# Optimization experiments

Measured on AMD Instinct MI355X. Metric: run time of the kernel, lower is better.

Reference implementation:

```python
import jax, jax.numpy as jnp
import numpy as np
from jax import lax

S = 2          # scale_factor
K = 5          # k_reassembly
KK = K * K     # 25 reassembly weights per output pixel


def _conv2d(x, w, b, pad):
    y = lax.conv_general_dilated(x, w, (1, 1), [(pad, pad), (pad, pad)],
                                 dimension_numbers=('NCHW', 'OIHW', 'NCHW'))
    return y + b[None, :, None, None]


def _pixel_shuffle(x, r):
    # (N, C*r*r, H, W) -> (N, C, H*r, W*r), torch PixelShuffle semantics
    n, crr, h, w = x.shape
    c = crr // (r * r)
    x = x.reshape(n, c, r, r, h, w)
    x = x.transpose(0, 1, 4, 2, 5, 3)
    return x.reshape(n, c, h * r, w * r)


def setup_inputs() -> dict:
    key = jax.random.key(0)
    k1, k2, k3 = jax.random.split(key, 3)
    x = jax.random.normal(k1, (4, 256, 64, 64), dtype=jnp.float32)
    w_comp = jax.random.normal(k2, (64, 256, 1, 1), dtype=jnp.float32) * 0.05
    b_comp = jnp.zeros((64,), dtype=jnp.float32)
    w_enc = jax.random.normal(k3, (S * S * KK, 64, 3, 3), dtype=jnp.float32) * 0.05
    b_enc = jnp.zeros((S * S * KK,), dtype=jnp.float32)
    return {"x": x, "w_comp": w_comp, "b_comp": b_comp, "w_enc": w_enc, "b_enc": b_enc}


def reference(x, w_comp, b_comp, w_enc, b_enc):
    N, C, H, W = x.shape
    p = K // 2
    # kernel prediction branch
    compressed = _conv2d(x, w_comp, b_comp, pad=0)                 # (N, 64, H, W)
    kernels = _conv2d(compressed, w_enc, b_enc, pad=1)             # (N, S*S*KK, H, W)
    kernels = _pixel_shuffle(kernels, S)                           # (N, KK, H*S, W*S)
    kernels = jax.nn.softmax(kernels, axis=1)
    # regroup kernels: (N, KK, Hs, Ws) -> (N, H, W, KK, S*S)  (torch unfold order: kh then kw)
    k_unf = kernels.reshape(N, KK, H, S, W, S)
    k_unf = k_unf.transpose(0, 2, 4, 1, 3, 5).reshape(N, H, W, KK, S * S)
    # gather KxK input patches: (N, C, H, W, KK), flattened (ih, iw) with ih outer
    xp = jnp.pad(x, ((0, 0), (0, 0), (p, p), (p, p)))
    patches = jnp.stack([xp[:, :, i:i + H, j:j + W]
                         for i in range(K) for j in range(K)], axis=-1)
    # weighted reassembly: per-pixel (C, KK) @ (KK, S*S)
    out = jnp.einsum('nchwk,nhwkq->nhwcq', patches, k_unf)          # (N, H, W, C, S*S)
    out = out.reshape(N, H, W, C * S * S).transpose(0, 3, 1, 2)     # (N, C*S*S, H, W)
    return _pixel_shuffle(out, S)                                   # (N, C, H*S, W*S)
```

## Files before the change

kernel.cpp:

```cpp
#include <hip/hip_runtime.h>
#include <hip/hip_fp16.h>

#define NB 4
#define CI 256
#define HH 64
#define WW 64
#define MC 64
#define HS 128
#define WS_ 128
#define HW 4096

typedef __attribute__((ext_vector_type(8))) short short8v;
typedef __attribute__((ext_vector_type(4))) float floatx4;

__device__ inline unsigned short f2bf(float f) {
  union { float f; unsigned u; } v; v.f = f;
  unsigned r = v.u + 0x7FFFu + ((v.u >> 16) & 1u);
  return (unsigned short)(r >> 16);
}

__global__ __launch_bounds__(256) void prep_kernel(
    const float* __restrict__ w_comp, const float* __restrict__ w_enc,
    unsigned short* __restrict__ Aw1, unsigned short* __restrict__ Aw2) {
  int i = blockIdx.x * 256 + threadIdx.x;
  if (i < 16384) {
    int kl = i & 31, o = (i >> 5) & 63, ks = i >> 11;
    Aw1[i] = f2bf(w_comp[o * 256 + ks * 32 + kl]);
  } else if (i < 16384 + 64512) {
    int j = i - 16384;
    int kl = j & 31, o = (j >> 5) % 112, ks = (j >> 5) / 112;
    int t = ks >> 1, m = (ks & 1) * 32 + kl;
    Aw2[j] = (o < 100) ? f2bf(w_enc[o * 576 + m * 9 + t]) : (unsigned short)0;
  }
}

__global__ __launch_bounds__(512, 1) void conv1x1_mfma(
    const float* __restrict__ x, const unsigned short* __restrict__ Aw1,
    const float* __restrict__ b_comp, unsigned short* __restrict__ comp_cl) {
  __shared__ float pacc[2][64][49];
  int tid = threadIdx.x;
  int wid = tid >> 6, lane = tid & 63;
  int tileid = wid & 1, kh = wid >> 1;
  int Nt = blockIdx.x * 2 + tileid;
  int n = Nt >> 8, pixbase = (Nt & 255) * 16;
  int l15 = lane & 15, g = lane >> 4;
  int pix = pixbase + l15;

  floatx4 acc[4];
#pragma unroll
  for (int ot = 0; ot < 4; ++ot) acc[ot] = (floatx4){0.f, 0.f, 0.f, 0.f};

  const float* xb = x + (size_t)n * CI * HW + pix;
  const unsigned short* ab = Aw1 + l15 * 32 + g * 8;

#pragma unroll
  for (int s = 0; s < 2; ++s) {
    int ks = kh * 2 + s;
    int c0 = ks * 32 + g * 8;
    short8v bfrag;
#pragma unroll
    for (int j = 0; j < 8; ++j)
      bfrag[j] = (short)f2bf(xb[(size_t)(c0 + j) * HW]);
#pragma unroll
    for (int ot = 0; ot < 4; ++ot) {
      short8v af = *(const short8v*)(ab + (ks * 64 + ot * 16) * 32);
      acc[ot] = __builtin_amdgcn_mfma_f32_16x16x32_bf16(af, bfrag, acc[ot], 0, 0, 0);
    }
  }

  if (kh > 0) {
#pragma unroll
    for (int ot = 0; ot < 4; ++ot)
#pragma unroll
      for (int r = 0; r < 4; ++r)
        pacc[tileid][lane][(kh - 1) * 16 + ot * 4 + r] = acc[ot][r];
  }
  __syncthreads();
  if (kh == 0) {
    unsigned short* cp = comp_cl + ((size_t)(n * HW + pix)) * 64;
#pragma unroll
    for (int ot = 0; ot < 4; ++ot) {
      const float4 bv = *(const float4*)(b_comp + ot * 16 + g * 4);
      float v0 = acc[ot][0] + bv.x, v1 = acc[ot][1] + bv.y;
      float v2 = acc[ot][2] + bv.z, v3 = acc[ot][3] + bv.w;
#pragma unroll
      for (int sl = 0; sl < 3; ++sl) {
        v0 += pacc[tileid][lane][sl * 16 + ot * 4 + 0];
        v1 += pacc[tileid][lane][sl * 16 + ot * 4 + 1];
        v2 += pacc[tileid][lane][sl * 16 + ot * 4 + 2];
        v3 += pacc[tileid][lane][sl * 16 + ot * 4 + 3];
      }
      unsigned h01 = (unsigned)f2bf(v0) | ((unsigned)f2bf(v1) << 16);
      unsigned h23 = (unsigned)f2bf(v2) | ((unsigned)f2bf(v3) << 16);
      *(int2*)(cp + ot * 16 + g * 4) = make_int2((int)h01, (int)h23);
    }
  }
}

#define TAPP(W, V, fa, fb)                                                     \
  asm("v_fma_mix_f32 %0, %1, %2, %0 op_sel:[0,0,0] op_sel_hi:[1,0,0]"          \
      : "+v"(a00) : "v"(W), "v"(fa));                                          \
  asm("v_fma_mix_f32 %0, %1, %2, %0 op_sel:[1,0,0] op_sel_hi:[1,0,0]"          \
      : "+v"(a01) : "v"(W), "v"(fa));                                          \
  asm("v_fma_mix_f32 %0, %1, %2, %0 op_sel:[0,0,0] op_sel_hi:[1,0,0]"          \
      : "+v"(a10) : "v"(V), "v"(fb));                                          \
  asm("v_fma_mix_f32 %0, %1, %2, %0 op_sel:[1,0,0] op_sel_hi:[1,0,0]"          \
      : "+v"(a11) : "v"(V), "v"(fb));

#define ROWP(WA, WB, WC, WD, WE, VA, VB, VC, VD, VE, RP)                       \
  { const float* rr = (RP);                                                    \
    float2 f01 = *(const float2*)(rr);                                         \
    float2 f23 = *(const float2*)(rr + 2);                                     \
    float2 f45 = *(const float2*)(rr + 4);                                     \
    TAPP(WA, VA, f01.x, f01.y) TAPP(WB, VB, f01.y, f23.x)                      \
    TAPP(WC, VC, f23.x, f23.y) TAPP(WD, VD, f23.y, f45.x)                      \
    TAPP(WE, VE, f45.x, f45.y) }

__device__ __forceinline__ float4 load_slot20(const float* __restrict__ xb,
                                              int h0, int w0, int f,
                                              bool interior) {
  int c = f / 30, rem = f - c * 30, r = rem / 5, h = rem - r * 5;
  int gh = h0 - 2 + r, gw = w0 - 2 + h * 4;
  if (interior) {
    const float* gp = xb + (size_t)c * HW + gh * WW + gw;
    float2 lo = *(const float2*)gp;
    float2 hi = *(const float2*)(gp + 2);
    return make_float4(lo.x, lo.y, hi.x, hi.y);
  }
  int ghc = min(max(gh, 0), 63);
  const float* rowp = xb + (size_t)c * HW + ghc * WW;
  float v0 = rowp[min(max(gw + 0, 0), 63)];
  float v1 = rowp[min(max(gw + 1, 0), 63)];
  float v2 = rowp[min(max(gw + 2, 0), 63)];
  float v3 = rowp[min(max(gw + 3, 0), 63)];
  bool rok = ((unsigned)gh < 64u);
  v0 = (rok && (unsigned)(gw + 0) < 64u) ? v0 : 0.f;
  v1 = (rok && (unsigned)(gw + 1) < 64u) ? v1 : 0.f;
  v2 = (rok && (unsigned)(gw + 2) < 64u) ? v2 : 0.f;
  v3 = (rok && (unsigned)(gw + 3) < 64u) ? v3 : 0.f;
  return make_float4(v0, v1, v2, v3);
}

__global__ __launch_bounds__(512, 4) void fused_kernel(
    const float* __restrict__ x,
    const unsigned short* __restrict__ comp_cl,
    const unsigned short* __restrict__ Aw2,
    const float* __restrict__ b_enc,
    float* __restrict__ out) {
  __shared__ float smem[12672];
  float* paccF = smem;
  float* xp = smem;
  unsigned int* wlds = (unsigned int*)(smem + 10880);

  int tid = threadIdx.x;
  int bid = blockIdx.x;
  int tile = bid & 127, n = bid >> 7;
  int tyi = tile >> 2, txi = tile & 3;
  int ty0 = tyi * 4, tx0 = txi * 32;
  int h0 = tyi * 2, w0 = txi * 16;

  int wid = tid >> 6, lane = tid & 63;
  int tileid = wid & 1, kh = wid >> 1;
  int l15 = lane & 15, g = lane >> 4;

  {
    int pix = (h0 + tileid) * 64 + w0 + l15;
    int y = pix >> 6, xcol = pix & 63;

    bool vm[9];
    int sh9[9];
#pragma unroll
    for (int t = 0; t < 9; ++t) {
      int dy = t / 3, dx = t % 3;
      vm[t] = ((unsigned)(y + dy - 1) < 64u) && ((unsigned)(xcol + dx - 1) < 64u);
      sh9[t] = (dy - 1) * 64 + (dx - 1);
    }

    floatx4 acc[7];
#pragma unroll
    for (int ot = 0; ot < 7; ++ot) acc[ot] = (floatx4){0.f, 0.f, 0.f, 0.f};

    const unsigned short* cb = comp_cl + (size_t)n * HW * 64;
    const unsigned short* ab = Aw2 + l15 * 32 + g * 8;
    const short8v zv = {0, 0, 0, 0, 0, 0, 0, 0};

    int ks0 = (kh < 2) ? kh * 5 : 10 + (kh - 2) * 4;
    int len = (kh < 2) ? 5 : 4;
#pragma unroll
    for (int s = 0; s < 5; ++s) {
      if (s < len) {
        int ks = ks0 + s;
        int t = ks >> 1, mh = ks & 1;
        const unsigned short* bp = cb + (pix + sh9[t]) * 64 + mh * 32 + g * 8;
        short8v bfrag = vm[t] ? *(const short8v*)bp : zv;
#pragma unroll
        for (int ot = 0; ot < 7; ++ot) {
          short8v af = *(const short8v*)(ab + (ks * 112 + ot * 16) * 32);
          acc[ot] = __builtin_amdgcn_mfma_f32_16x16x32_bf16(af, bfrag, acc[ot], 0, 0, 0);
        }
      }
    }

    if (kh > 0) {
#pragma unroll
      for (int ot = 0; ot < 7; ++ot)
#pragma unroll
        for (int r = 0; r < 4; ++r)
          paccF[(tileid * 64 + lane) * 85 + (kh - 1) * 28 + ot * 4 + r] =
              acc[ot][r];
    }
    __syncthreads();
    if (kh == 0) {
#pragma unroll
      for (int ot = 0; ot < 7; ++ot) {
        int ob = ot * 16 + g * 4; if (ob > 96) ob = 96;
        const float4 bv = *(const float4*)(b_enc + ob);
        acc[ot][0] += bv.x; acc[ot][1] += bv.y;
        acc[ot][2] += bv.z; acc[ot][3] += bv.w;
#pragma unroll
        for (int sl = 0; sl < 3; ++sl) {
          acc[ot][0] += paccF[(tileid * 64 + lane) * 85 + sl * 28 + ot * 4 + 0];
          acc[ot][1] += paccF[(tileid * 64 + lane) * 85 + sl * 28 + ot * 4 + 1];
          acc[ot][2] += paccF[(tileid * 64 + lane) * 85 + sl * 28 + ot * 4 + 2];
          acc[ot][3] += paccF[(tileid * 64 + lane) * 85 + sl * 28 + ot * 4 + 3];
        }
      }

#pragma unroll
      for (int r = 0; r < 4; ++r) {
        float m = acc[0][r];
#pragma unroll
        for (int ot = 1; ot < 6; ++ot) m = fmaxf(m, acc[ot][r]);
        if (g == 0) m = fmaxf(m, acc[6][r]);
        m = fmaxf(m, __shfl_xor(m, 16));
        m = fmaxf(m, __shfl_xor(m, 32));
        float s = 0.f;
        float e[7];
#pragma unroll
        for (int ot = 0; ot < 7; ++ot) {
          bool val = (ot < 6) || (g == 0);
          e[ot] = val ? __expf(acc[ot][r] - m) : 0.f;
          s += e[ot];
        }
        s += __shfl_xor(s, 16);
        s += __shfl_xor(s, 32);
        float inv = 1.f / s;
#pragma unroll
        for (int ot = 0; ot < 7; ++ot) acc[ot][r] = e[ot] * inv;
      }

#pragma unroll
      for (int sh = 0; sh < 2; ++sh) {
        unsigned int* wq = wlds + sh * 896 + tileid * 448 + l15 * 28;
#pragma unroll
        for (int ot = 0; ot < 7; ++ot) {
          if ((ot < 6) || (g == 0)) {
            __half2 h2 = __floats2half2_rn(acc[ot][2 * sh], acc[ot][2 * sh + 1]);
            wq[ot * 4 + g] = *reinterpret_cast<unsigned int*>(&h2);
          }
        }
      }
    }
  }
  __syncthreads();

  int cslot = tid >> 5;
  int rem = tid & 31;
  int py = rem >> 4;
  int shsel = (rem >> 3) & 1;
  int pxp = rem & 7;
  int oy = ty0 + 2 * py + shsel;
  int ox0 = tx0 + 4 * pxp;
  int cb0 = 2 * pxp;

  const unsigned int* wtA = wlds + shsel * 896 + py * 448 + cb0 * 28;
  const unsigned int* wtB = wtA + 28;
  uint4 A0 = *(const uint4*)(wtA + 0);
  uint4 A1 = *(const uint4*)(wtA + 4);
  uint4 A2 = *(const uint4*)(wtA + 8);
  uint4 A3 = *(const uint4*)(wtA + 12);
  uint4 A4 = *(const uint4*)(wtA + 16);
  uint4 A5 = *(const uint4*)(wtA + 20);
  unsigned int A6 = wtA[24];
  uint4 B0 = *(const uint4*)(wtB + 0);
  uint4 B1 = *(const uint4*)(wtB + 4);
  uint4 B2 = *(const uint4*)(wtB + 8);
  uint4 B3 = *(const uint4*)(wtB + 12);
  uint4 B4 = *(const uint4*)(wtB + 16);
  uint4 B5 = *(const uint4*)(wtB + 20);
  unsigned int B6 = wtB[24];

  bool interior = (tyi >= 1) && (tyi <= 30) && (txi >= 1) && (txi <= 2);
  bool extra = tid < 384;

  for (int cs = 0; cs < 4; ++cs) {
    const float* xb = x + (size_t)(n * CI + cs * 64) * HW;
    float4 s0 = load_slot20(xb, h0, w0, tid,        interior);
    float4 s1 = load_slot20(xb, h0, w0, tid + 512,  interior);
    float4 s2 = load_slot20(xb, h0, w0, tid + 1024, interior);
    float4 s3 = extra ? load_slot20(xb, h0, w0, tid + 1536, interior)
                      : make_float4(0.f, 0.f, 0.f, 0.f);
    if (cs > 0) __syncthreads();
    *(float4*)(xp + 4 * (tid))        = s0;
    *(float4*)(xp + 4 * (tid + 512))  = s1;
    *(float4*)(xp + 4 * (tid + 1024)) = s2;
    if (extra) *(float4*)(xp + 4 * (tid + 1536)) = s3;
    __syncthreads();

    float* outb = out + ((size_t)(n * CI + cs * 64) * HS + oy) * WS_ + ox0;
#pragma unroll
    for (int it = 0; it < 4; ++it) {
      int cl = it * 16 + cslot;
      const float* p = xp + cl * 120 + py * 20 + cb0;
      float a00 = 0.f, a01 = 0.f, a10 = 0.f, a11 = 0.f;
      ROWP(A0.x, A0.y, A0.z, A0.w, A1.x, B0.x, B0.y, B0.z, B0.w, B1.x, p)
      ROWP(A1.y, A1.z, A1.w, A2.x, A2.y, B1.y, B1.z, B1.w, B2.x, B2.y, p + 20)
      ROWP(A2.z, A2.w, A3.x, A3.y, A3.z, B2.z, B2.w, B3.x, B3.y, B3.z, p + 40)
      ROWP(A3.w, A4.x, A4.y, A4.z, A4.w, B3.w, B4.x, B4.y, B4.z, B4.w, p + 60)
      ROWP(A5.x, A5.y, A5.z, A5.w, A6,   B5.x, B5.y, B5.z, B5.w, B6,   p + 80)
      *(float4*)(outb + (size_t)cl * HS * WS_) = make_float4(a00, a01, a10, a11);
    }
  }
}

extern "C" void kernel_launch(void* const* d_in, const int* in_sizes, int n_in,
                              void* d_out, int out_size, void* d_ws,
                              size_t ws_size, hipStream_t stream) {
  const float* x      = (const float*)d_in[0];
  const float* w_comp = (const float*)d_in[1];
  const float* b_comp = (const float*)d_in[2];
  const float* w_enc  = (const float*)d_in[3];
  const float* b_enc  = (const float*)d_in[4];
  float* out = (float*)d_out;

  char* ws = (char*)d_ws;
  unsigned short* comp_cl = (unsigned short*)ws;
  unsigned short* Aw1     = (unsigned short*)(ws + 2097152);
  unsigned short* Aw2     = (unsigned short*)(ws + 2129920);

  prep_kernel<<<dim3(316), 256, 0, stream>>>(w_comp, w_enc, Aw1, Aw2);
  conv1x1_mfma<<<dim3(512), 512, 0, stream>>>(x, Aw1, b_comp, comp_cl);
  fused_kernel<<<dim3(512), 512, 0, stream>>>(x, comp_cl, Aw2, b_enc, out);
}
```

Measured before the change: 58.16 us.

## Shrink fused tile to 2x8 low-res pixels with 256-thread blocks

Halves the spatial tile of the fused encoder/reassembly kernel from 2x16 to 2x8 input pixels, using 256-thread blocks and twice as many blocks. The MFMA fragment now packs two 8-pixel rows into one 16-column tile, and the halo staging, LDS layout and thread mapping are rewritten for the narrower 12-wide halo. This is meant to improve load balance and occupancy (1024 blocks, smaller LDS). In exchange it raises the halo overhead per output pixel and re-reads more neighbouring input data.

Result: slower. 68.37 us (+17.6%).

```diff
diff --git a/kernel.cpp b/kernel.cpp
--- a/kernel.cpp
+++ b/kernel.cpp
@@ -116,10 +116,10 @@
     TAPP(WC, VC, f23.x, f23.y) TAPP(WD, VD, f23.y, f45.x)                      \
     TAPP(WE, VE, f45.x, f45.y) }
 
-__device__ __forceinline__ float4 load_slot20(const float* __restrict__ xb,
+__device__ __forceinline__ float4 load_slot18(const float* __restrict__ xb,
                                               int h0, int w0, int f,
                                               bool interior) {
-  int c = f / 30, rem = f - c * 30, r = rem / 5, h = rem - r * 5;
+  int c = f / 18, rem = f - c * 18, r = rem / 3, h = rem - r * 3;
   int gh = h0 - 2 + r, gw = w0 - 2 + h * 4;
   if (interior) {
     const float* gp = xb + (size_t)c * HW + gh * WW + gw;
@@ -141,30 +141,29 @@
   return make_float4(v0, v1, v2, v3);
 }
 
-__global__ __launch_bounds__(512, 4) void fused_kernel(
+__global__ __launch_bounds__(256, 2) void fused_kernel(
     const float* __restrict__ x,
     const unsigned short* __restrict__ comp_cl,
     const unsigned short* __restrict__ Aw2,
     const float* __restrict__ b_enc,
     float* __restrict__ out) {
-  __shared__ float smem[12672];
+  __shared__ float smem[6336];
   float* paccF = smem;
   float* xp = smem;
-  unsigned int* wlds = (unsigned int*)(smem + 10880);
+  unsigned int* wlds = (unsigned int*)(smem + 5440);
 
   int tid = threadIdx.x;
   int bid = blockIdx.x;
-  int tile = bid & 127, n = bid >> 7;
-  int tyi = tile >> 2, txi = tile & 3;
-  int ty0 = tyi * 4, tx0 = txi * 32;
-  int h0 = tyi * 2, w0 = txi * 16;
-
-  int wid = tid >> 6, lane = tid & 63;
-  int tileid = wid & 1, kh = wid >> 1;
+  int tile = bid & 255, n = bid >> 8;
+  int tyi = tile >> 3, txi = tile & 7;
+  int ty0 = tyi * 4, tx0 = txi * 16;
+  int h0 = tyi * 2, w0 = txi * 8;
+
+  int kh = tid >> 6, lane = tid & 63;
   int l15 = lane & 15, g = lane >> 4;
 
   {
-    int pix = (h0 + tileid) * 64 + w0 + l15;
+    int pix = (h0 + (l15 >> 3)) * 64 + w0 + (l15 & 7);
     int y = pix >> 6, xcol = pix & 63;
 
     bool vm[9];
@@ -206,8 +205,7 @@
       for (int ot = 0; ot < 7; ++ot)
 #pragma unroll
         for (int r = 0; r < 4; ++r)
-          paccF[(tileid * 64 + lane) * 85 + (kh - 1) * 28 + ot * 4 + r] =
-              acc[ot][r];
+          paccF[lane * 85 + (kh - 1) * 28 + ot * 4 + r] = acc[ot][r];
     }
     __syncthreads();
     if (kh == 0) {
@@ -219,10 +217,10 @@
         acc[ot][2] += bv.z; acc[ot][3] += bv.w;
 #pragma unroll
         for (int sl = 0; sl < 3; ++sl) {
-          acc[ot][0] += paccF[(tileid * 64 + lane) * 85 + sl * 28 + ot * 4 + 0];
-          acc[ot][1] += paccF[(tileid * 64 + lane) * 85 + sl * 28 + ot * 4 + 1];
-          acc[ot][2] += paccF[(tileid * 64 + lane) * 85 + sl * 28 + ot * 4 + 2];
-          acc[ot][3] += paccF[(tileid * 64 + lane) * 85 + sl * 28 + ot * 4 + 3];
+          acc[ot][0] += paccF[lane * 85 + sl * 28 + ot * 4 + 0];
+          acc[ot][1] += paccF[lane * 85 + sl * 28 + ot * 4 + 1];
+          acc[ot][2] += paccF[lane * 85 + sl * 28 + ot * 4 + 2];
+          acc[ot][3] += paccF[lane * 85 + sl * 28 + ot * 4 + 3];
         }
       }
 
@@ -251,7 +249,7 @@
 
 #pragma unroll
       for (int sh = 0; sh < 2; ++sh) {
-        unsigned int* wq = wlds + sh * 896 + tileid * 448 + l15 * 28;
+        unsigned int* wq = wlds + sh * 448 + l15 * 28;
 #pragma unroll
         for (int ot = 0; ot < 7; ++ot) {
           if ((ot < 6) || (g == 0)) {
@@ -264,16 +262,16 @@
   }
   __syncthreads();
 
-  int cslot = tid >> 5;
-  int rem = tid & 31;
-  int py = rem >> 4;
-  int shsel = (rem >> 3) & 1;
-  int pxp = rem & 7;
+  int cslot = tid >> 4;
+  int rem = tid & 15;
+  int py = rem >> 3;
+  int shsel = (rem >> 2) & 1;
+  int pxp = rem & 3;
   int oy = ty0 + 2 * py + shsel;
   int ox0 = tx0 + 4 * pxp;
   int cb0 = 2 * pxp;
 
-  const unsigned int* wtA = wlds + shsel * 896 + py * 448 + cb0 * 28;
+  const unsigned int* wtA = wlds + shsel * 448 + (py * 8 + 2 * pxp) * 28;
   const unsigned int* wtB = wtA + 28;
   uint4 A0 = *(const uint4*)(wtA + 0);
   uint4 A1 = *(const uint4*)(wtA + 4);
@@ -290,34 +288,36 @@
   uint4 B5 = *(const uint4*)(wtB + 20);
   unsigned int B6 = wtB[24];
 
-  bool interior = (tyi >= 1) && (tyi <= 30) && (txi >= 1) && (txi <= 2);
-  bool extra = tid < 384;
+  bool interior = (tyi >= 1) && (tyi <= 30) && (txi >= 1) && (txi <= 6);
+  bool halfv = tid < 128;
 
   for (int cs = 0; cs < 4; ++cs) {
     const float* xb = x + (size_t)(n * CI + cs * 64) * HW;
-    float4 s0 = load_slot20(xb, h0, w0, tid,        interior);
-    float4 s1 = load_slot20(xb, h0, w0, tid + 512,  interior);
-    float4 s2 = load_slot20(xb, h0, w0, tid + 1024, interior);
-    float4 s3 = extra ? load_slot20(xb, h0, w0, tid + 1536, interior)
+    float4 s0 = load_slot18(xb, h0, w0, tid,        interior);
+    float4 s1 = load_slot18(xb, h0, w0, tid + 256,  interior);
+    float4 s2 = load_slot18(xb, h0, w0, tid + 512,  interior);
+    float4 s3 = load_slot18(xb, h0, w0, tid + 768,  interior);
+    float4 s4 = halfv ? load_slot18(xb, h0, w0, tid + 1024, interior)
                       : make_float4(0.f, 0.f, 0.f, 0.f);
     if (cs > 0) __syncthreads();
     *(float4*)(xp + 4 * (tid))        = s0;
-    *(float4*)(xp + 4 * (tid + 512))  = s1;
-    *(float4*)(xp + 4 * (tid + 1024)) = s2;
-    if (extra) *(float4*)(xp + 4 * (tid + 1536)) = s3;
+    *(float4*)(xp + 4 * (tid + 256))  = s1;
+    *(float4*)(xp + 4 * (tid + 512))  = s2;
+    *(float4*)(xp + 4 * (tid + 768))  = s3;
+    if (halfv) *(float4*)(xp + 4 * (tid + 1024)) = s4;
     __syncthreads();
 
     float* outb = out + ((size_t)(n * CI + cs * 64) * HS + oy) * WS_ + ox0;
 #pragma unroll
     for (int it = 0; it < 4; ++it) {
       int cl = it * 16 + cslot;
-      const float* p = xp + cl * 120 + py * 20 + cb0;
+      const float* p = xp + cl * 72 + py * 12 + cb0;
       float a00 = 0.f, a01 = 0.f, a10 = 0.f, a11 = 0.f;
       ROWP(A0.x, A0.y, A0.z, A0.w, A1.x, B0.x, B0.y, B0.z, B0.w, B1.x, p)
-      ROWP(A1.y, A1.z, A1.w, A2.x, A2.y, B1.y, B1.z, B1.w, B2.x, B2.y, p + 20)
-      ROWP(A2.z, A2.w, A3.x, A3.y, A3.z, B2.z, B2.w, B3.x, B3.y, B3.z, p + 40)
-      ROWP(A3.w, A4.x, A4.y, A4.z, A4.w, B3.w, B4.x, B4.y, B4.z, B4.w, p + 60)
-      ROWP(A5.x, A5.y, A5.z, A5.w, A6,   B5.x, B5.y, B5.z, B5.w, B6,   p + 80)
+      ROWP(A1.y, A1.z, A1.w, A2.x, A2.y, B1.y, B1.z, B1.w, B2.x, B2.y, p + 12)
+      ROWP(A2.z, A2.w, A3.x, A3.y, A3.z, B2.z, B2.w, B3.x, B3.y, B3.z, p + 24)
+      ROWP(A3.w, A4.x, A4.y, A4.z, A4.w, B3.w, B4.x, B4.y, B4.z, B4.w, p + 36)
+      ROWP(A5.x, A5.y, A5.z, A5.w, A6,   B5.x, B5.y, B5.z, B5.w, B6,   p + 48)
       *(float4*)(outb + (size_t)cl * HS * WS_) = make_float4(a00, a01, a10, a11);
     }
   }
@@ -340,5 +340,5 @@
 
   prep_kernel<<<dim3(316), 256, 0, stream>>>(w_comp, w_enc, Aw1, Aw2);
   conv1x1_mfma<<<dim3(512), 512, 0, stream>>>(x, Aw1, b_comp, comp_cl);
-  fused_kernel<<<dim3(512), 512, 0, stream>>>(x, comp_cl, Aw2, b_enc, out);
-}
+  fused_kernel<<<dim3(1024), 256, 0, stream>>>(x, comp_cl, Aw2, b_enc, out);
+}
```

## Double-buffer input channel tiles in LDS to overlap global loads with reassembly

Applied to the files above, without the earlier changes.

Splits the channel loop into 8 chunks of 32 channels held in two alternating LDS buffers. The next chunk's global loads are issued before computing on the current chunk and are written to the other buffer afterward, leaving one barrier per iteration instead of two. This is meant to hide global load latency behind the reassembly math, at the cost of more loop iterations and more registers live across the compute.

New measurement: 55.34 us. 1.05x faster.

```diff
diff --git a/kernel.cpp b/kernel.cpp
--- a/kernel.cpp
+++ b/kernel.cpp
@@ -149,7 +149,6 @@
     float* __restrict__ out) {
   __shared__ float smem[12672];
   float* paccF = smem;
-  float* xp = smem;
   unsigned int* wlds = (unsigned int*)(smem + 10880);
 
   int tid = threadIdx.x;
@@ -291,27 +290,36 @@
   unsigned int B6 = wtB[24];
 
   bool interior = (tyi >= 1) && (tyi <= 30) && (txi >= 1) && (txi <= 2);
-  bool extra = tid < 384;
-
-  for (int cs = 0; cs < 4; ++cs) {
-    const float* xb = x + (size_t)(n * CI + cs * 64) * HW;
-    float4 s0 = load_slot20(xb, h0, w0, tid,        interior);
-    float4 s1 = load_slot20(xb, h0, w0, tid + 512,  interior);
-    float4 s2 = load_slot20(xb, h0, w0, tid + 1024, interior);
-    float4 s3 = extra ? load_slot20(xb, h0, w0, tid + 1536, interior)
+  bool extra = tid < 448;
+
+  {
+    const float* xb = x + (size_t)(n * CI) * HW;
+    float4 s0 = load_slot20(xb, h0, w0, tid, interior);
+    float4 s1 = extra ? load_slot20(xb, h0, w0, tid + 512, interior)
                       : make_float4(0.f, 0.f, 0.f, 0.f);
-    if (cs > 0) __syncthreads();
-    *(float4*)(xp + 4 * (tid))        = s0;
-    *(float4*)(xp + 4 * (tid + 512))  = s1;
-    *(float4*)(xp + 4 * (tid + 1024)) = s2;
-    if (extra) *(float4*)(xp + 4 * (tid + 1536)) = s3;
-    __syncthreads();
-
-    float* outb = out + ((size_t)(n * CI + cs * 64) * HS + oy) * WS_ + ox0;
-#pragma unroll
-    for (int it = 0; it < 4; ++it) {
+    float* xpb = smem;
+    *(float4*)(xpb + 4 * tid) = s0;
+    if (extra) *(float4*)(xpb + 4 * (tid + 512)) = s1;
+  }
+  __syncthreads();
+
+  for (int cs = 0; cs < 8; ++cs) {
+    float* xpcur = smem + (cs & 1) * 3840;
+    float* xpnxt = smem + ((cs + 1) & 1) * 3840;
+
+    float4 t0 = make_float4(0.f, 0.f, 0.f, 0.f);
+    float4 t1 = make_float4(0.f, 0.f, 0.f, 0.f);
+    if (cs < 7) {
+      const float* xbn = x + (size_t)(n * CI + (cs + 1) * 32) * HW;
+      t0 = load_slot20(xbn, h0, w0, tid, interior);
+      if (extra) t1 = load_slot20(xbn, h0, w0, tid + 512, interior);
+    }
+
+    float* outb = out + ((size_t)(n * CI + cs * 32) * HS + oy) * WS_ + ox0;
+#pragma unroll
+    for (int it = 0; it < 2; ++it) {
       int cl = it * 16 + cslot;
-      const float* p = xp + cl * 120 + py * 20 + cb0;
+      const float* p = xpcur + cl * 120 + py * 20 + cb0;
       float a00 = 0.f, a01 = 0.f, a10 = 0.f, a11 = 0.f;
       ROWP(A0.x, A0.y, A0.z, A0.w, A1.x, B0.x, B0.y, B0.z, B0.w, B1.x, p)
       ROWP(A1.y, A1.z, A1.w, A2.x, A2.y, B1.y, B1.z, B1.w, B2.x, B2.y, p + 20)
@@ -319,6 +327,12 @@
       ROWP(A3.w, A4.x, A4.y, A4.z, A4.w, B3.w, B4.x, B4.y, B4.z, B4.w, p + 60)
       ROWP(A5.x, A5.y, A5.z, A5.w, A6,   B5.x, B5.y, B5.z, B5.w, B6,   p + 80)
       *(float4*)(outb + (size_t)cl * HS * WS_) = make_float4(a00, a01, a10, a11);
+    }
+
+    if (cs < 7) {
+      *(float4*)(xpnxt + 4 * tid) = t0;
+      if (extra) *(float4*)(xpnxt + 4 * (tid + 512)) = t1;
+      __syncthreads();
     }
   }
 }
```
